# Kernel tuning notes

Measured on AMD Instinct MI355X. Metric: run time of the kernel, lower is better.

## Reference

```python
import jax, jax.numpy as jnp
import numpy as np

D_MODEL = 512
D_STATE = 16
EXPAND = 2
DT_RANK = 8
D_INNER = EXPAND * D_MODEL  # 1024
LN_EPS = 1e-5


def setup_inputs() -> dict:
    key = jax.random.key(0)
    ks = jax.random.split(key, 10)
    B, H, W = 8, 48, 48
    inp = {
        "x": jax.random.normal(ks[0], (B, H, W, D_MODEL), jnp.float32),
        # Linear weights stored [in, out] (torch weight transposed)
        "W_in": jax.random.normal(ks[1], (D_MODEL, 2 * D_INNER), jnp.float32) * 0.02,
        # depthwise conv kernel, HWIO with feature_group_count = D_INNER
        "conv_k": jax.random.normal(ks[2], (3, 3, 1, D_INNER), jnp.float32) * 0.1,
        "W_xproj": jax.random.normal(ks[3], (D_INNER, DT_RANK + 2 * D_STATE), jnp.float32) * 0.02,
        "W_dt": jax.random.uniform(ks[4], (DT_RANK, D_INNER), jnp.float32, -0.1, 0.1),
        "b_dt": jnp.full((D_INNER,), 0.1, jnp.float32),
        "A_log": jax.random.normal(ks[5], (D_STATE,), jnp.float32) * 0.02,
        "Dskip": jnp.ones((D_INNER,), jnp.float32),
        "W_dtN": jax.random.normal(ks[6], (D_INNER, D_STATE), jnp.float32) * 0.02,
        "b_dtN": jnp.zeros((D_STATE,), jnp.float32),
        "ln_g": jnp.ones((D_INNER,), jnp.float32),
        "ln_b": jnp.zeros((D_INNER,), jnp.float32),
        "W_out": jax.random.normal(ks[7], (D_INNER, D_MODEL), jnp.float32) * 0.02,
        "b_out": jnp.zeros((D_MODEL,), jnp.float32),
    }
    return inp


def _ss2d(x, W_in, conv_k, W_xproj, W_dt, b_dt, A_log, Dskip, W_dtN, b_dtN,
          ln_g, ln_b, W_out, b_out):
    B, H, W_, _ = x.shape
    L = H * W_
    # in_proj and split into x / gate z
    xz = x @ W_in                                   # [B,H,W,2*D_INNER]
    xh, z = jnp.split(xz, 2, axis=-1)
    # depthwise 3x3 conv (NHWC)
    xc = jax.lax.conv_general_dilated(
        xh, conv_k, window_strides=(1, 1), padding='SAME',
        dimension_numbers=('NHWC', 'HWIO', 'NHWC'),
        feature_group_count=D_INNER)                 # [B,H,W,D_INNER]
    # x_proj -> (dt_rank, B, C)
    xp = xc @ W_xproj
    dt_r = xp[..., :DT_RANK]
    Bp = xp[..., DT_RANK:DT_RANK + D_STATE]
    Cp = xp[..., DT_RANK + D_STATE:]
    dt = dt_r @ W_dt + b_dt                          # [B,H,W,D_INNER]
    # flatten spatial dims into sequence
    x_seq = xc.reshape(B, L, D_INNER)
    dt_seq = jax.nn.softplus(dt.reshape(B, L, D_INNER))
    B_seq = Bp.reshape(B, L, D_STATE)
    C_seq = Cp.reshape(B, L, D_STATE)
    A = -jnp.exp(A_log)                              # [N]; A_log expanded over D is constant per-row
    dtN = dt_seq @ W_dtN + b_dtN                     # dt_to_N_proj(softplus(dt)) -> [B,L,N]

    def step(h, t):
        x_t, dt_t, dtN_t, B_t, C_t = t               # [B,D],[B,D],[B,N],[B,N],[B,N]
        dA = jnp.exp(dt_t[:, :, None] * A)           # [B,D,N]
        dB = dtN_t * B_t                             # [B,N]
        h = dA * h + dB[:, None, :] * x_t[:, :, None]  # [B,D,N]
        y = jnp.einsum('bdn,bn->bd', h, C_t) + Dskip * x_t
        return h, y

    h0 = jnp.zeros((B, D_INNER, D_STATE), x.dtype)
    xs = (x_seq.transpose(1, 0, 2), dt_seq.transpose(1, 0, 2),
          dtN.transpose(1, 0, 2), B_seq.transpose(1, 0, 2),
          C_seq.transpose(1, 0, 2))
    _, ys = jax.lax.scan(step, h0, xs)               # ys: [L,B,D]
    y = ys.transpose(1, 0, 2).reshape(B, H, W_, D_INNER)
    # LayerNorm over channel dim
    mu = y.mean(-1, keepdims=True)
    var = ((y - mu) ** 2).mean(-1, keepdims=True)
    y = (y - mu) / jnp.sqrt(var + LN_EPS) * ln_g + ln_b
    # gate and out projection (dropout = identity in eval)
    y = y * jax.nn.silu(z)
    return y @ W_out + b_out


def reference(x, W_in, conv_k, W_xproj, W_dt, b_dt, A_log, Dskip, W_dtN,
              b_dtN, ln_g, ln_b, W_out, b_out):
    return _ss2d(x, W_in, conv_k, W_xproj, W_dt, b_dt, A_log, Dskip, W_dtN,
                 b_dtN, ln_g, ln_b, W_out, b_out)
```

## Files before the change

### kernel.cpp

```cpp
#include <hip/hip_runtime.h>
#include <hip/hip_bf16.h>

#define NBATCH 8
#define HEIGHT 48
#define WIDTH  48
#define DMODEL 512
#define DSTATE 16
#define DTRANK 8
#define DINNER 1024
#define LSEQ   (HEIGHT*WIDTH)
#define NROWS  (NBATCH*LSEQ)
#define NXP    40
#define NCH    64
#define TCH    36

typedef unsigned short u16;
typedef unsigned int   u32;
typedef __attribute__((ext_vector_type(8))) short short8;
typedef __attribute__((ext_vector_type(4))) float f32x4;

__device__ __forceinline__ float bf2f(u16 u) {
    u32 x = ((u32)u) << 16;
    return __uint_as_float(x);
}
__device__ __forceinline__ u16 f2bf(float f) {
    u32 x = __float_as_uint(f);
    u32 r = (x + 0x7FFFu + ((x >> 16) & 1u)) >> 16;
    return (u16)r;
}

#if __has_builtin(__builtin_amdgcn_exp2f)
__device__ __forceinline__ float EXP2(float x) { return __builtin_amdgcn_exp2f(x); }
#else
__device__ __forceinline__ float EXP2(float x) { return __expf(x * 0.69314718f); }
#endif

__device__ __forceinline__ float* pslot(float* pz, size_t i) {
    return pz + ((i >> 9) << 10) + (i & 511);
}

#define GLD16(g, l) __builtin_amdgcn_global_load_lds( \
    (const __attribute__((address_space(1))) void*)(g), \
    (__attribute__((address_space(3))) void*)(l), 16, 0, 0)

__global__ __launch_bounds__(256) void k_prep_x(const float* __restrict__ x,
                                                u16* __restrict__ xbf) {
    int i = blockIdx.x * 256 + threadIdx.x;
    float4 v = *reinterpret_cast<const float4*>(x + (size_t)i * 4);
    ushort4 o;
    o.x = f2bf(v.x); o.y = f2bf(v.y); o.z = f2bf(v.z); o.w = f2bf(v.w);
    *reinterpret_cast<ushort4*>(xbf + (size_t)i * 4) = o;
}

__global__ __launch_bounds__(256) void k_prep_w(const float* __restrict__ W_in,
                                                const float* __restrict__ W_out,
                                                const float* __restrict__ W_xproj,
                                                const float* __restrict__ W_dtN,
                                                u16* __restrict__ WinT,
                                                u16* __restrict__ WoutT,
                                                u16* __restrict__ WxpB,
                                                u16* __restrict__ WdtNB) {
    int idx = blockIdx.x * 256 + threadIdx.x;
    if (idx < 2048 * 512) {
        int n = idx >> 9, k = idx & 511;
        WinT[idx] = f2bf(W_in[(size_t)k * 2048 + n]);
    } else if (idx < 2048 * 512 + 512 * 1024) {
        int j = idx - 2048 * 512;
        int n = j >> 10, k = j & 1023;
        WoutT[j] = f2bf(W_out[(size_t)k * 512 + n]);
    } else if (idx < 2048 * 512 + 512 * 1024 + 48 * 1024) {
        int j = idx - (2048 * 512 + 512 * 1024);
        int n = j >> 10, k = j & 1023;
        WxpB[j] = (n < NXP) ? f2bf(W_xproj[(size_t)k * NXP + n]) : (u16)0;
    } else {
        int j = idx - (2048 * 512 + 512 * 1024 + 48 * 1024);
        int n = j >> 10, k = j & 1023;
        WdtNB[j] = f2bf(W_dtN[(size_t)k * DSTATE + n]);
    }
}

template<int K, int LDA, int LDB, int LDC, bool F32OUT>
__global__ __launch_bounds__(256) void k_gemm_mfma(const u16* __restrict__ A,
                                                   const u16* __restrict__ B,
                                                   const float* __restrict__ bias,
                                                   void* __restrict__ Cv) {
    __shared__ u16 As[128 * 32];
    __shared__ u16 Bs[128 * 32];
    const int tid = threadIdx.x;
    const int l   = tid & 63;
    const int w   = tid >> 6;
    const int wm  = w >> 1, wn = w & 1;
    const int m0  = blockIdx.y * 128, n0 = blockIdx.x * 128;
    const int srow = w * 32 + (l >> 2);
    const int sc   = l & 3;
    const int kh = l >> 4;
    const int lr = l & 15;

    f32x4 acc[4][4];
#pragma unroll
    for (int i = 0; i < 4; ++i)
#pragma unroll
        for (int j = 0; j < 4; ++j)
            acc[i][j] = (f32x4){0.f, 0.f, 0.f, 0.f};

    for (int k0 = 0; k0 < K; k0 += 32) {
#pragma unroll
        for (int i = 0; i < 2; ++i) {
            int r  = srow + i * 16;
            int cg = sc ^ ((r >> 1) & 3);
            const u16* ga = A + (size_t)(m0 + r) * LDA + k0 + cg * 8;
            const u16* gb = B + (size_t)(n0 + r) * LDB + k0 + cg * 8;
            GLD16(ga, As + (w * 2 + i) * 512);
            GLD16(gb, Bs + (w * 2 + i) * 512);
        }
        __syncthreads();
        short8 af[4], bfr[4];
#pragma unroll
        for (int f = 0; f < 4; ++f) {
            int ar = wm * 64 + f * 16 + lr;
            af[f]  = *reinterpret_cast<const short8*>(As + ar * 32 + ((kh ^ ((ar >> 1) & 3)) * 8));
            int br = wn * 64 + f * 16 + lr;
            bfr[f] = *reinterpret_cast<const short8*>(Bs + br * 32 + ((kh ^ ((br >> 1) & 3)) * 8));
        }
#pragma unroll
        for (int fm = 0; fm < 4; ++fm)
#pragma unroll
            for (int fn = 0; fn < 4; ++fn)
                acc[fm][fn] = __builtin_amdgcn_mfma_f32_16x16x32_bf16(
                    af[fm], bfr[fn], acc[fm][fn], 0, 0, 0);
        __syncthreads();
    }

#pragma unroll
    for (int fm = 0; fm < 4; ++fm) {
#pragma unroll
        for (int r = 0; r < 4; ++r) {
            int row = m0 + wm * 64 + fm * 16 + (l >> 4) * 4 + r;
#pragma unroll
            for (int fn = 0; fn < 4; ++fn) {
                int col = n0 + wn * 64 + fn * 16 + lr;
                if (F32OUT) {
                    ((float*)Cv)[(size_t)row * LDC + col] = acc[fm][fn][r] + bias[col];
                } else {
                    ((u16*)Cv)[(size_t)row * LDC + col] = f2bf(acc[fm][fn][r]);
                }
            }
        }
    }
}

__global__ __launch_bounds__(256) void k_conv(const u16* __restrict__ xz,
                                              const float* __restrict__ ck,
                                              u16* __restrict__ xc) {
    int row = blockIdx.x;
    int w = row % WIDTH;
    int hb = row / WIDTH;
    int h = hb % HEIGHT;
    int b = hb / HEIGHT;
    int c0 = threadIdx.x * 4;
    float a0 = 0.f, a1 = 0.f, a2 = 0.f, a3 = 0.f;
#pragma unroll
    for (int kh = 0; kh < 3; ++kh) {
        int hh = h + kh - 1;
        if (hh < 0 || hh >= HEIGHT) continue;
#pragma unroll
        for (int kw = 0; kw < 3; ++kw) {
            int ww = w + kw - 1;
            if (ww < 0 || ww >= WIDTH) continue;
            int r = (b * HEIGHT + hh) * WIDTH + ww;
            ushort4 v = *reinterpret_cast<const ushort4*>(xz + (size_t)r * 2048 + c0);
            float4 kv = *reinterpret_cast<const float4*>(ck + (kh * 3 + kw) * DINNER + c0);
            a0 = fmaf(bf2f(v.x), kv.x, a0);
            a1 = fmaf(bf2f(v.y), kv.y, a1);
            a2 = fmaf(bf2f(v.z), kv.z, a2);
            a3 = fmaf(bf2f(v.w), kv.w, a3);
        }
    }
    ushort4 ov;
    ov.x = f2bf(a0); ov.y = f2bf(a1); ov.z = f2bf(a2); ov.w = f2bf(a3);
    *reinterpret_cast<ushort4*>(xc + (size_t)row * DINNER + c0) = ov;
}

__global__ __launch_bounds__(256) void k_xproj(const u16* __restrict__ xc,
                                               const u16* __restrict__ WxpB,
                                               float* __restrict__ xp_out) {
    __shared__ u16 As[64 * 32];
    __shared__ u16 Bs[48 * 32];
    const int tid = threadIdx.x;
    const int l = tid & 63;
    const int w = tid >> 6;
    const int m0 = blockIdx.x * 64;
    const int kh = l >> 4, lr = l & 15;
    const int srow = w * 16 + (l >> 2);
    const int sc = l & 3;

    f32x4 acc[3];
    acc[0] = acc[1] = acc[2] = (f32x4){0.f, 0.f, 0.f, 0.f};

    for (int k0 = 0; k0 < 1024; k0 += 32) {
        {
            int cg = sc ^ ((srow >> 1) & 3);
            GLD16(xc + (size_t)(m0 + srow) * DINNER + k0 + cg * 8, As + w * 512);
            if (w < 3)
                GLD16(WxpB + (size_t)srow * 1024 + k0 + cg * 8, Bs + w * 512);
        }
        __syncthreads();
        int ar = w * 16 + lr;
        short8 af = *reinterpret_cast<const short8*>(As + ar * 32 + ((kh ^ ((ar >> 1) & 3)) * 8));
#pragma unroll
        for (int fn = 0; fn < 3; ++fn) {
            int br = fn * 16 + lr;
            short8 bf = *reinterpret_cast<const short8*>(Bs + br * 32 + ((kh ^ ((br >> 1) & 3)) * 8));
            acc[fn] = __builtin_amdgcn_mfma_f32_16x16x32_bf16(af, bf, acc[fn], 0, 0, 0);
        }
        __syncthreads();
    }
#pragma unroll
    for (int fn = 0; fn < 3; ++fn)
#pragma unroll
        for (int r = 0; r < 4; ++r) {
            int row = m0 + w * 16 + (l >> 4) * 4 + r;
            int col = fn * 16 + lr;
            if (col < NXP) xp_out[(size_t)row * NXP + col] = acc[fn][r];
        }
}

__global__ __launch_bounds__(256) void k_dt(const float* __restrict__ xp,
                                            const float* __restrict__ W_dt,
                                            const float* __restrict__ b_dt,
                                            u16* __restrict__ dt_out) {
    int gid = blockIdx.x * 256 + threadIdx.x;
    int row = gid >> 7;
    int dj  = (gid & 127) * 8;
    const float* xr = xp + (size_t)row * NXP;
    float4 xa = *reinterpret_cast<const float4*>(xr);
    float4 xb = *reinterpret_cast<const float4*>(xr + 4);
    float xv[8] = {xa.x, xa.y, xa.z, xa.w, xb.x, xb.y, xb.z, xb.w};
    float a[8];
    {
        float4 b0 = *reinterpret_cast<const float4*>(b_dt + dj);
        float4 b1 = *reinterpret_cast<const float4*>(b_dt + dj + 4);
        a[0]=b0.x; a[1]=b0.y; a[2]=b0.z; a[3]=b0.w;
        a[4]=b1.x; a[5]=b1.y; a[6]=b1.z; a[7]=b1.w;
    }
#pragma unroll
    for (int j = 0; j < 8; ++j) {
        float4 w0 = *reinterpret_cast<const float4*>(W_dt + j * DINNER + dj);
        float4 w1 = *reinterpret_cast<const float4*>(W_dt + j * DINNER + dj + 4);
        a[0] = fmaf(xv[j], w0.x, a[0]); a[1] = fmaf(xv[j], w0.y, a[1]);
        a[2] = fmaf(xv[j], w0.z, a[2]); a[3] = fmaf(xv[j], w0.w, a[3]);
        a[4] = fmaf(xv[j], w1.x, a[4]); a[5] = fmaf(xv[j], w1.y, a[5]);
        a[6] = fmaf(xv[j], w1.z, a[6]); a[7] = fmaf(xv[j], w1.w, a[7]);
    }
    short8 o;
#pragma unroll
    for (int j = 0; j < 8; ++j) {
        float dt = fmaxf(a[j], 0.f) + log1pf(__expf(-fabsf(a[j])));
        o[j] = (short)f2bf(dt);
    }
    *reinterpret_cast<short8*>(dt_out + (size_t)row * DINNER + dj) = o;
}

__global__ __launch_bounds__(256) void k_dtn(const u16* __restrict__ dtb,
                                             const u16* __restrict__ WdtNB,
                                             const float* __restrict__ b_dtN,
                                             const float* __restrict__ xp,
                                             float* __restrict__ dnBC) {
    __shared__ u16 As[64 * 32];
    __shared__ u16 Bs[16 * 32];
    const int tid = threadIdx.x;
    const int l = tid & 63;
    const int w = tid >> 6;
    const int m0 = blockIdx.x * 64;
    const int kh = l >> 4, lr = l & 15;
    const int srow = w * 16 + (l >> 2);
    const int sc = l & 3;

    f32x4 acc = (f32x4){0.f, 0.f, 0.f, 0.f};

    for (int k0 = 0; k0 < 1024; k0 += 32) {
        {
            int cg = sc ^ ((srow >> 1) & 3);
            GLD16(dtb + (size_t)(m0 + srow) * DINNER + k0 + cg * 8, As + w * 512);
            if (w == 0)
                GLD16(WdtNB + (size_t)srow * 1024 + k0 + cg * 8, Bs);
        }
        __syncthreads();
        int ar = w * 16 + lr;
        short8 af = *reinterpret_cast<const short8*>(As + ar * 32 + ((kh ^ ((ar >> 1) & 3)) * 8));
        short8 bf = *reinterpret_cast<const short8*>(Bs + lr * 32 + ((kh ^ ((lr >> 1) & 3)) * 8));
        acc = __builtin_amdgcn_mfma_f32_16x16x32_bf16(af, bf, acc, 0, 0, 0);
        __syncthreads();
    }
    float bn = b_dtN[lr];
#pragma unroll
    for (int r = 0; r < 4; ++r) {
        int row = m0 + w * 16 + (l >> 4) * 4 + r;
        float dn = acc[r] + bn;
        float Bv = xp[(size_t)row * NXP + DTRANK + lr];
        float Cv = xp[(size_t)row * NXP + DTRANK + DSTATE + lr];
        dnBC[(size_t)row * 32 + lr]      = dn * Bv;
        dnBC[(size_t)row * 32 + 16 + lr] = Cv;
    }
}

__global__ __launch_bounds__(256) void k_scan_p1(const u16* __restrict__ xc,
                                                 const u16* __restrict__ dtb,
                                                 const float* __restrict__ dnBC,
                                                 const float* __restrict__ A_log,
                                                 float* __restrict__ Pz,
                                                 float* __restrict__ Qbuf) {
    const int tid = threadIdx.x;
    const int blk = blockIdx.x;
    const int quarter = blk & 3;
    const int bc = blk >> 2;
    const int c = bc & (NCH - 1);
    const int b = bc >> 6;
    const int d = quarter * 256 + tid;

    float An2[16];
#pragma unroll
    for (int n = 0; n < 16; ++n)
        An2[n] = -__expf(A_log[n]) * 1.44269504f;

    float h[16];
#pragma unroll
    for (int n = 0; n < 16; ++n) h[n] = 0.f;
    float sdt = 0.f;

    const size_t row0 = (size_t)b * LSEQ + (size_t)c * TCH;
#pragma unroll 4
    for (int t = 0; t < TCH; ++t) {
        size_t row = row0 + t;
        float dt = bf2f(dtb[row * DINNER + d]);
        float xt = bf2f(xc[row * DINNER + d]);
        const float4* dv = reinterpret_cast<const float4*>(dnBC + row * 32);
        float4 u0 = dv[0], u1 = dv[1], u2 = dv[2], u3 = dv[3];
        sdt += dt;
        float u[16] = {u0.x,u0.y,u0.z,u0.w, u1.x,u1.y,u1.z,u1.w,
                       u2.x,u2.y,u2.z,u2.w, u3.x,u3.y,u3.z,u3.w};
#pragma unroll
        for (int n = 0; n < 16; ++n) {
            float dA = EXP2(dt * An2[n]);
            h[n] = fmaf(dA, h[n], u[n] * xt);
        }
    }
    size_t base = ((size_t)bc << 14) + d;
#pragma unroll
    for (int n = 0; n < 16; ++n) {
        *pslot(Pz, base + (size_t)n * DINNER) = EXP2(sdt * An2[n]);
        Qbuf[base + (size_t)n * DINNER] = h[n];
    }
}

__global__ __launch_bounds__(256) void k_scan_p2(const float* __restrict__ Pz,
                                                 float* __restrict__ Qbuf) {
    int tid = blockIdx.x * 256 + threadIdx.x;
    int b = tid >> 14, rem = tid & 16383;
    float h = 0.f;
    for (int c = 0; c < NCH; ++c) {
        size_t idx = ((size_t)(b * NCH + c) << 14) + rem;
        float P = *pslot(const_cast<float*>(Pz), idx);
        float q = Qbuf[idx];
        Qbuf[idx] = h;
        h = fmaf(P, h, q);
    }
}

__global__ __launch_bounds__(256) void k_scan_p3(const u16* __restrict__ xc,
                                                 const u16* __restrict__ dtb,
                                                 const float* __restrict__ dnBC,
                                                 const float* __restrict__ A_log,
                                                 const float* __restrict__ Dskip,
                                                 const float* __restrict__ Qbuf,
                                                 u16* __restrict__ ybuf) {
    const int tid = threadIdx.x;
    const int blk = blockIdx.x;
    const int quarter = blk & 3;
    const int bc = blk >> 2;
    const int c = bc & (NCH - 1);
    const int b = bc >> 6;
    const int d = quarter * 256 + tid;

    float An2[16];
#pragma unroll
    for (int n = 0; n < 16; ++n)
        An2[n] = -__expf(A_log[n]) * 1.44269504f;

    float h[16];
    size_t base = ((size_t)bc << 14) + d;
#pragma unroll
    for (int n = 0; n < 16; ++n) h[n] = Qbuf[base + (size_t)n * DINNER];
    float Dsk = Dskip[d];

    const size_t row0 = (size_t)b * LSEQ + (size_t)c * TCH;
#pragma unroll 2
    for (int t = 0; t < TCH; ++t) {
        size_t row = row0 + t;
        float dt = bf2f(dtb[row * DINNER + d]);
        float xt = bf2f(xc[row * DINNER + d]);
        const float4* sv = reinterpret_cast<const float4*>(dnBC + row * 32);
        float4 u0 = sv[0], u1 = sv[1], u2 = sv[2], u3 = sv[3];
        float4 c0 = sv[4], c1 = sv[5], c2 = sv[6], c3 = sv[7];
        float u[16]  = {u0.x,u0.y,u0.z,u0.w, u1.x,u1.y,u1.z,u1.w,
                        u2.x,u2.y,u2.z,u2.w, u3.x,u3.y,u3.z,u3.w};
        float cv[16] = {c0.x,c0.y,c0.z,c0.w, c1.x,c1.y,c1.z,c1.w,
                        c2.x,c2.y,c2.z,c2.w, c3.x,c3.y,c3.z,c3.w};
        float ys[4] = {Dsk * xt, 0.f, 0.f, 0.f};
#pragma unroll
        for (int n = 0; n < 16; ++n) {
            float dA = EXP2(dt * An2[n]);
            h[n] = fmaf(dA, h[n], u[n] * xt);
            ys[n & 3] = fmaf(h[n], cv[n], ys[n & 3]);
        }
        ybuf[row * 2048 + d] = f2bf((ys[0] + ys[1]) + (ys[2] + ys[3]));
    }
}

__global__ __launch_bounds__(256) void k_ln_gate(u16* __restrict__ xz,
                                                 const float* __restrict__ ln_g,
                                                 const float* __restrict__ ln_b) {
    __shared__ float red[8];
    int row = blockIdx.x, tid = threadIdx.x;
    u16* yrow = xz + (size_t)row * 2048;
    int c0 = tid * 4;
    ushort4 v = *reinterpret_cast<const ushort4*>(yrow + c0);
    float y0 = bf2f(v.x), y1 = bf2f(v.y), y2 = bf2f(v.z), y3 = bf2f(v.w);
    float s = y0 + y1 + y2 + y3;
    float q = y0 * y0 + y1 * y1 + y2 * y2 + y3 * y3;
#pragma unroll
    for (int m = 32; m; m >>= 1) {
        s += __shfl_xor(s, m, 64);
        q += __shfl_xor(q, m, 64);
    }
    int lane = tid & 63, wv = tid >> 6;
    if (lane == 0) { red[wv] = s; red[4 + wv] = q; }
    __syncthreads();
    s = red[0] + red[1] + red[2] + red[3];
    q = red[4] + red[5] + red[6] + red[7];
    float mu = s * (1.f / DINNER);
    float var = q * (1.f / DINNER) - mu * mu;
    float rstd = rsqrtf(var + 1e-5f);
    ushort4 zv = *reinterpret_cast<const ushort4*>(yrow + DINNER + c0);
    float4 lg = *reinterpret_cast<const float4*>(ln_g + c0);
    float4 lb = *reinterpret_cast<const float4*>(ln_b + c0);
    float z0 = bf2f(zv.x), z1 = bf2f(zv.y), z2 = bf2f(zv.z), z3 = bf2f(zv.w);
    float g0 = ((y0 - mu) * rstd * lg.x + lb.x) * (z0 / (1.f + __expf(-z0)));
    float g1 = ((y1 - mu) * rstd * lg.y + lb.y) * (z1 / (1.f + __expf(-z1)));
    float g2 = ((y2 - mu) * rstd * lg.z + lb.z) * (z2 / (1.f + __expf(-z2)));
    float g3 = ((y3 - mu) * rstd * lg.w + lb.w) * (z3 / (1.f + __expf(-z3)));
    ushort4 ov;
    ov.x = f2bf(g0); ov.y = f2bf(g1); ov.z = f2bf(g2); ov.w = f2bf(g3);
    *reinterpret_cast<ushort4*>(yrow + c0) = ov;
}

extern "C" void kernel_launch(void* const* d_in, const int* in_sizes, int n_in,
                              void* d_out, int out_size, void* d_ws, size_t ws_size,
                              hipStream_t stream) {
    const float* x       = (const float*)d_in[0];
    const float* W_in    = (const float*)d_in[1];
    const float* conv_k  = (const float*)d_in[2];
    const float* W_xproj = (const float*)d_in[3];
    const float* W_dt    = (const float*)d_in[4];
    const float* b_dt    = (const float*)d_in[5];
    const float* A_log   = (const float*)d_in[6];
    const float* Dskip   = (const float*)d_in[7];
    const float* W_dtN   = (const float*)d_in[8];
    const float* b_dtN   = (const float*)d_in[9];
    const float* ln_g    = (const float*)d_in[10];
    const float* ln_b    = (const float*)d_in[11];
    const float* W_out   = (const float*)d_in[12];
    const float* b_out   = (const float*)d_in[13];
    float* out = (float*)d_out;

    char* ws = (char*)d_ws;
    size_t off = 0;
    u16*   xz    = (u16*)(ws + off); off += (size_t)NROWS * 2048 * 2;
    u16*   xc    = (u16*)(ws + off); off += (size_t)NROWS * 1024 * 2;
    u16*   dtb   = (u16*)(ws + off); off += (size_t)NROWS * 1024 * 2;
    float* xpb   = (float*)(ws + off); off += (size_t)NROWS * NXP * 4;
    float* dnBC  = (float*)(ws + off); off += (size_t)NROWS * 32 * 4;
    char*  scr   = ws + off; off += (size_t)NBATCH * NCH * DINNER * DSTATE * 4;
    u16*   xbf   = (u16*)scr;
    float* Qbuf  = (float*)scr;
    float* Pz    = (float*)xz;
    u16*   WinT  = (u16*)(ws + off); off += (size_t)2048 * 512 * 2;
    u16*   WoutT = (u16*)(ws + off); off += (size_t)512 * 1024 * 2;
    u16*   WxpB  = (u16*)(ws + off); off += (size_t)48 * 1024 * 2;
    u16*   WdtNB = (u16*)(ws + off); off += (size_t)16 * 1024 * 2;

    k_prep_x<<<(NROWS * DMODEL / 4) / 256, 256, 0, stream>>>(x, xbf);
    k_prep_w<<<(2048 * 512 + 512 * 1024 + 48 * 1024 + 16 * 1024) / 256, 256, 0, stream>>>(
        W_in, W_out, W_xproj, W_dtN, WinT, WoutT, WxpB, WdtNB);
    k_gemm_mfma<512, 512, 512, 2048, false>
        <<<dim3(2048 / 128, NROWS / 128), 256, 0, stream>>>(xbf, WinT, nullptr, xz);
    k_conv<<<NROWS, 256, 0, stream>>>(xz, conv_k, xc);
    k_xproj<<<NROWS / 64, 256, 0, stream>>>(xc, WxpB, xpb);
    k_dt<<<(NROWS * DINNER / 8) / 256, 256, 0, stream>>>(xpb, W_dt, b_dt, dtb);
    k_dtn<<<NROWS / 64, 256, 0, stream>>>(dtb, WdtNB, b_dtN, xpb, dnBC);
    k_scan_p1<<<NBATCH * NCH * 4, 256, 0, stream>>>(xc, dtb, dnBC, A_log,
                                                    Pz, Qbuf);
    k_scan_p2<<<(NBATCH * DINNER * DSTATE) / 256, 256, 0, stream>>>(Pz, Qbuf);
    k_scan_p3<<<NBATCH * NCH * 4, 256, 0, stream>>>(xc, dtb, dnBC, A_log,
                                                    Dskip, Qbuf, xz);
    k_ln_gate<<<NROWS, 256, 0, stream>>>(xz, ln_g, ln_b);
    k_gemm_mfma<1024, 2048, 1024, 512, true>
        <<<dim3(DMODEL / 128, NROWS / 128), 256, 0, stream>>>(xz, WoutT, b_out, out);
}
```

Baseline: 371.6 us.

## Store per-chunk dt sums instead of decay products and swizzle workgroups across XCDs

The first scan pass now writes one summed dt per (batch, chunk, channel) instead of sixteen precomputed decay factors. The second pass recomputes the decay with exp2 from that sum and A_log. This cuts the scratch traffic for the decay term by a factor of sixteen, at the cost of extra exp work in the serial pass. Workgroup ids in the GEMMs and the scan passes are also remapped with an XCD-style round-robin swizzle, so neighbouring tiles share L2 on the same chiplet. The sum buffer reuses the xproj buffer, which is safe only because xpb is no longer read after the dtn kernel.

```diff
diff --git a/kernel.cpp b/kernel.cpp
--- a/kernel.cpp
+++ b/kernel.cpp
@@ -34,10 +34,6 @@
 #else
 __device__ __forceinline__ float EXP2(float x) { return __expf(x * 0.69314718f); }
 #endif
-
-__device__ __forceinline__ float* pslot(float* pz, size_t i) {
-    return pz + ((i >> 9) << 10) + (i & 511);
-}
 
 #define GLD16(g, l) __builtin_amdgcn_global_load_lds( \
     (const __attribute__((address_space(1))) void*)(g), \
@@ -90,7 +86,12 @@
     const int l   = tid & 63;
     const int w   = tid >> 6;
     const int wm  = w >> 1, wn = w & 1;
-    const int m0  = blockIdx.y * 128, n0 = blockIdx.x * 128;
+    const int id   = blockIdx.y * gridDim.x + blockIdx.x;
+    const int nwg  = gridDim.x * gridDim.y;
+    const int swz  = (id & 7) * (nwg >> 3) + (id >> 3);
+    const int bx   = swz % gridDim.x;
+    const int by   = swz / gridDim.x;
+    const int m0  = by * 128, n0 = bx * 128;
     const int srow = w * 32 + (l >> 2);
     const int sc   = l & 3;
     const int kh = l >> 4;
@@ -308,12 +309,13 @@
                                                  const u16* __restrict__ dtb,
                                                  const float* __restrict__ dnBC,
                                                  const float* __restrict__ A_log,
-                                                 float* __restrict__ Pz,
+                                                 float* __restrict__ sdt_out,
                                                  float* __restrict__ Qbuf) {
     const int tid = threadIdx.x;
-    const int blk = blockIdx.x;
-    const int quarter = blk & 3;
-    const int bc = blk >> 2;
+    const int id  = blockIdx.x;
+    const int swz = (id & 7) * ((NBATCH * NCH * 4) >> 3) + (id >> 3);
+    const int quarter = swz & 3;
+    const int bc = swz >> 2;
     const int c = bc & (NCH - 1);
     const int b = bc >> 6;
     const int d = quarter * 256 + tid;
@@ -345,22 +347,25 @@
             h[n] = fmaf(dA, h[n], u[n] * xt);
         }
     }
+    sdt_out[(size_t)bc * DINNER + d] = sdt;
     size_t base = ((size_t)bc << 14) + d;
 #pragma unroll
-    for (int n = 0; n < 16; ++n) {
-        *pslot(Pz, base + (size_t)n * DINNER) = EXP2(sdt * An2[n]);
+    for (int n = 0; n < 16; ++n)
         Qbuf[base + (size_t)n * DINNER] = h[n];
-    }
-}
-
-__global__ __launch_bounds__(256) void k_scan_p2(const float* __restrict__ Pz,
+}
+
+__global__ __launch_bounds__(256) void k_scan_p2(const float* __restrict__ sdt,
+                                                 const float* __restrict__ A_log,
                                                  float* __restrict__ Qbuf) {
     int tid = blockIdx.x * 256 + threadIdx.x;
     int b = tid >> 14, rem = tid & 16383;
+    int n = rem >> 10, d = rem & 1023;
+    float An2 = -__expf(A_log[n]) * 1.44269504f;
     float h = 0.f;
     for (int c = 0; c < NCH; ++c) {
-        size_t idx = ((size_t)(b * NCH + c) << 14) + rem;
-        float P = *pslot(const_cast<float*>(Pz), idx);
+        int bc = b * NCH + c;
+        float P = EXP2(sdt[(size_t)bc * DINNER + d] * An2);
+        size_t idx = ((size_t)bc << 14) + rem;
         float q = Qbuf[idx];
         Qbuf[idx] = h;
         h = fmaf(P, h, q);
@@ -375,9 +380,10 @@
                                                  const float* __restrict__ Qbuf,
                                                  u16* __restrict__ ybuf) {
     const int tid = threadIdx.x;
-    const int blk = blockIdx.x;
-    const int quarter = blk & 3;
-    const int bc = blk >> 2;
+    const int id  = blockIdx.x;
+    const int swz = (id & 7) * ((NBATCH * NCH * 4) >> 3) + (id >> 3);
+    const int quarter = swz & 3;
+    const int bc = swz >> 2;
     const int c = bc & (NCH - 1);
     const int b = bc >> 6;
     const int d = quarter * 256 + tid;
@@ -483,7 +489,7 @@
     char*  scr   = ws + off; off += (size_t)NBATCH * NCH * DINNER * DSTATE * 4;
     u16*   xbf   = (u16*)scr;
     float* Qbuf  = (float*)scr;
-    float* Pz    = (float*)xz;
+    float* sdtb  = xpb;
     u16*   WinT  = (u16*)(ws + off); off += (size_t)2048 * 512 * 2;
     u16*   WoutT = (u16*)(ws + off); off += (size_t)512 * 1024 * 2;
     u16*   WxpB  = (u16*)(ws + off); off += (size_t)48 * 1024 * 2;
@@ -499,8 +505,8 @@
     k_dt<<<(NROWS * DINNER / 8) / 256, 256, 0, stream>>>(xpb, W_dt, b_dt, dtb);
     k_dtn<<<NROWS / 64, 256, 0, stream>>>(dtb, WdtNB, b_dtN, xpb, dnBC);
     k_scan_p1<<<NBATCH * NCH * 4, 256, 0, stream>>>(xc, dtb, dnBC, A_log,
-                                                    Pz, Qbuf);
-    k_scan_p2<<<(NBATCH * DINNER * DSTATE) / 256, 256, 0, stream>>>(Pz, Qbuf);
+                                                    sdtb, Qbuf);
+    k_scan_p2<<<(NBATCH * DINNER * DSTATE) / 256, 256, 0, stream>>>(sdtb, A_log, Qbuf);
     k_scan_p3<<<NBATCH * NCH * 4, 256, 0, stream>>>(xc, dtb, dnBC, A_log,
                                                     Dskip, Qbuf, xz);
     k_ln_gate<<<NROWS, 256, 0, stream>>>(xz, ln_g, ln_b);
```

Result: faster. 351.8 us (-5.3%).
